# Performance work log

Hardware: AMD Instinct MI355X
Metric: run time of the kernel (lower is better)

Reference implementation:

```python
import jax, jax.numpy as jnp
import numpy as np

V, H, I, L = 32000, 1024, 2048, 4
NH, NKV, HD = 16, 8, 64
E, K = 4, 2
B, S = 2, 1024
NEG = jnp.finfo(jnp.float32).min


def setup_inputs() -> dict:
    key = jax.random.key(0)
    ks = jax.random.split(key, 11)
    w = lambda k, shape: jax.random.normal(k, shape, jnp.float32) * 0.02
    return dict(
        input_ids=jax.random.randint(ks[0], (B, S), 0, V),
        embed=w(ks[1], (V, H)),
        Wq=w(ks[2], (L, H, NH * HD)),
        Wk=w(ks[3], (L, H, NKV * HD)),
        Wv=w(ks[4], (L, H, NKV * HD)),
        Wo=w(ks[5], (L, NH * HD, H)),
        ln1=jnp.ones((L, H), jnp.float32),
        ln2=jnp.ones((L, H), jnp.float32),
        gate=w(ks[6], (L, H, E)),
        Wg=w(ks[7], (L, E, H, I)),
        Wu=w(ks[8], (L, E, H, I)),
        Wd=w(ks[9], (L, E, I, H)),
        norm_w=jnp.ones((H,), jnp.float32),
        lm_head=w(ks[10], (H, V)),
    )


def rmsnorm(x, w, eps=1e-6):
    var = jnp.mean(x * x, axis=-1, keepdims=True)
    return w * (x * jax.lax.rsqrt(var + eps))


def forward(input_ids, embed, Wq, Wk, Wv, Wo, ln1, ln2, gate, Wg, Wu, Wd, norm_w, lm_head):
    b, s = input_ids.shape
    h = embed[input_ids]  # [B,S,H]
    mask = jnp.where(jnp.triu(jnp.ones((s, s), bool), 1), NEG, 0.0)[None, None]  # causal [1,1,S,S]
    inv_sqrt_hd = 1.0 / np.sqrt(HD)
    rep = NH // NKV

    def step(h, p):
        wq, wk, wv, wo, l1, l2, gw, wg, wu, wd = p
        x = rmsnorm(h, l1)
        q = (x @ wq).reshape(b, s, NH, HD).transpose(0, 2, 1, 3)    # [B,NH,S,HD]
        k = (x @ wk).reshape(b, s, NKV, HD).transpose(0, 2, 1, 3)   # [B,NKV,S,HD]
        v = (x @ wv).reshape(b, s, NKV, HD).transpose(0, 2, 1, 3)
        k = jnp.repeat(k, rep, axis=1)  # GQA repeat_kv
        v = jnp.repeat(v, rep, axis=1)
        scores = jnp.einsum('bhqd,bhkd->bhqk', q, k) * inv_sqrt_hd + mask
        attn = jax.nn.softmax(scores, axis=-1)
        o = jnp.einsum('bhqk,bhkd->bhqd', attn, v).transpose(0, 2, 1, 3).reshape(b, s, NH * HD)
        h = h + o @ wo
        # MoE FFN (top-k routing, combine via per-expert gate weights)
        x = rmsnorm(h, l2).reshape(b * s, H)              # [T,H]
        probs = jax.nn.softmax(x @ gw, axis=-1)           # [T,E]
        topk_p, topk_i = jax.lax.top_k(probs, K)          # [T,K]
        comb = jnp.sum(topk_p[..., None] * jax.nn.one_hot(topk_i, E, dtype=x.dtype), axis=1)  # [T,E]
        g = jax.nn.silu(jnp.einsum('th,ehi->eti', x, wg))  # [E,T,I]
        u = jnp.einsum('th,ehi->eti', x, wu)
        eo = jnp.einsum('eti,eih->eth', g * u, wd)         # [E,T,H]
        moe = jnp.einsum('eth,te->th', eo, comb).reshape(b, s, H)
        return h + moe, None

    h, _ = jax.lax.scan(step, h, (Wq, Wk, Wv, Wo, ln1, ln2, gate, Wg, Wu, Wd))
    return rmsnorm(h, norm_w) @ lm_head  # [B,S,V]


def reference(input_ids, embed, Wq, Wk, Wv, Wo, ln1, ln2, gate, Wg, Wu, Wd, norm_w, lm_head):
    return forward(input_ids, embed, Wq, Wk, Wv, Wo, ln1, ln2, gate, Wg, Wu, Wd, norm_w, lm_head)
```

## Files before the change

kernel.cpp:

```cpp
#include <hip/hip_runtime.h>

#define T_ 2048
#define H_ 1024
#define S_ 1024
#define V_ 32000
#define I_ 2048
#define NHD 1024
#define KVD 512

typedef unsigned short u16;
typedef unsigned int u32;
typedef __attribute__((ext_vector_type(8))) short s16x8;
typedef __attribute__((ext_vector_type(4))) float f32x4;

__device__ __forceinline__ u16 f2b(float f){ u32 x=__builtin_bit_cast(u32,f); return (u16)((x+0x7fffu+((x>>16)&1u))>>16); }
__device__ __forceinline__ float b2f(u16 u){ return __builtin_bit_cast(float,(u32)u<<16); }
__device__ __forceinline__ float wsum(float v){ for(int o=32;o;o>>=1) v+=__shfl_xor(v,o); return v; }

__device__ __forceinline__ void gl16(const void* g, void* l){
  __builtin_amdgcn_global_load_lds(
      (const __attribute__((address_space(1))) unsigned int*)g,
      (__attribute__((address_space(3))) unsigned int*)l, 16, 0, 0);
}

__global__ void k_embed(const int* __restrict__ ids, const float* __restrict__ emb,
                        float* __restrict__ h, int* __restrict__ cnt){
  if(blockIdx.x==0 && threadIdx.x<16) cnt[threadIdx.x]=0;
  int t = blockIdx.x;
  long src = (long)ids[t]*H_;
  ((float4*)(h + (long)t*H_))[threadIdx.x] = ((const float4*)(emb+src))[threadIdx.x];
}

__global__ void k_rms_sp(const float* __restrict__ h, const float* __restrict__ w,
                         u16* __restrict__ xhi, u16* __restrict__ xlo){
  int wid = threadIdx.x>>6, lane = threadIdx.x&63;
  int t = blockIdx.x*4 + wid;
  const float* row = h + (long)t*H_;
  float v[16]; float ss=0.f;
  #pragma unroll
  for(int j=0;j<16;j++){ v[j]=row[j*64+lane]; ss += v[j]*v[j]; }
  ss = wsum(ss);
  float rstd = rsqrtf(ss/(float)H_ + 1e-6f);
  #pragma unroll
  for(int j=0;j<16;j++){
    int idx=j*64+lane;
    float y = v[j]*rstd*w[idx];
    u16 hv = f2b(y);
    xhi[(long)t*H_+idx] = hv;
    if(xlo) xlo[(long)t*H_+idx] = f2b(y - b2f(hv));
  }
}

__global__ void k_router(const float* __restrict__ h, const float* __restrict__ lw,
                         const float* __restrict__ gate, float* __restrict__ comb,
                         int* __restrict__ lists, int* __restrict__ cnt, int2* __restrict__ epos,
                         u16* __restrict__ xhi, u16* __restrict__ xlo){
  int wid = threadIdx.x>>6, lane = threadIdx.x&63;
  int t = blockIdx.x*4+wid;
  const float* row = h + (long)t*H_;
  float v[16]; float ss=0.f;
  #pragma unroll
  for(int j=0;j<16;j++){ v[j]=row[j*64+lane]; ss+=v[j]*v[j]; }
  ss = wsum(ss);
  float rstd = rsqrtf(ss/(float)H_+1e-6f);
  float a0=0,a1=0,a2=0,a3=0;
  #pragma unroll
  for(int j=0;j<16;j++){
    int idx=j*64+lane;
    float y = v[j]*rstd*lw[idx];
    u16 hv = f2b(y);
    xhi[(long)t*H_+idx] = hv;
    xlo[(long)t*H_+idx] = f2b(y - b2f(hv));
    float4 g4 = ((const float4*)gate)[idx];
    a0 += y*g4.x; a1 += y*g4.y; a2 += y*g4.z; a3 += y*g4.w;
  }
  a0=wsum(a0); a1=wsum(a1); a2=wsum(a2); a3=wsum(a3);
  if(lane==0){
    float p[4]={a0,a1,a2,a3};
    float m = fmaxf(fmaxf(p[0],p[1]),fmaxf(p[2],p[3]));
    float s=0; for(int e=0;e<4;e++){ p[e]=__expf(p[e]-m); s+=p[e]; }
    for(int e=0;e<4;e++) p[e]/=s;
    int i1=0; for(int e=1;e<4;e++) if(p[e]>p[i1]) i1=e;
    int i2=-1; for(int e=0;e<4;e++){ if(e==i1) continue; if(i2<0||p[e]>p[i2]) i2=e; }
    float* c = comb + (long)t*4;
    for(int e=0;e<4;e++) c[e] = (e==i1||e==i2)? p[e] : 0.f;
    int p1 = atomicAdd(&cnt[i1],1); lists[i1*T_+p1]=t;
    int p2 = atomicAdd(&cnt[i2],1); lists[i2*T_+p2]=t;
    epos[t] = make_int2((p1<<2)|i1, (p2<<2)|i2);
  }
}

__global__ void k_transpose(const float* __restrict__ in, u16* __restrict__ hi, u16* __restrict__ lo,
                            int R, int C, long zi, long zo){
  __shared__ float tile[32][33];
  in += (long)blockIdx.z*zi; hi += (long)blockIdx.z*zo; if(lo) lo += (long)blockIdx.z*zo;
  int c0 = blockIdx.x*32, r0 = blockIdx.y*32;
  int tx = threadIdx.x, ty = threadIdx.y;
  #pragma unroll
  for(int i=0;i<4;i++) tile[ty+8*i][tx] = in[(long)(r0+ty+8*i)*C + c0+tx];
  __syncthreads();
  #pragma unroll
  for(int i=0;i<4;i++){
    int cc=ty+8*i; float v = tile[tx][cc];
    u16 hv = f2b(v);
    long idx = (long)(c0+cc)*R + r0+tx;
    hi[idx] = hv;
    if(lo) lo[idx] = f2b(v - b2f(hv));
  }
}

__global__ void k_wtrans(const float* __restrict__ Wq, const float* __restrict__ Wk,
                         const float* __restrict__ Wv, const float* __restrict__ Wo,
                         const float* __restrict__ Wg, const float* __restrict__ Wu,
                         const float* __restrict__ Wd,
                         u16* __restrict__ qkvh, u16* __restrict__ qkvl,
                         u16* __restrict__ oh, u16* __restrict__ ol,
                         u16* __restrict__ gh, u16* __restrict__ gl_,
                         u16* __restrict__ uh, u16* __restrict__ ul,
                         u16* __restrict__ dh, u16* __restrict__ dl)
{
  __shared__ float tile[32][33];
  int id = blockIdx.x;
  const float* in; u16 *hi, *lo; int R, C, bx, by;
  if(id < 1024){ in=Wq; hi=qkvh; lo=qkvl; R=1024; C=1024; bx=id&31; by=id>>5; }
  else if(id < 1536){ id-=1024; in=Wk; hi=qkvh+1048576; lo=qkvl+1048576; R=1024; C=512; bx=id&15; by=id>>4; }
  else if(id < 2048){ id-=1536; in=Wv; hi=qkvh+1572864; lo=qkvl+1572864; R=1024; C=512; bx=id&15; by=id>>4; }
  else if(id < 3072){ id-=2048; in=Wo; hi=oh; lo=ol; R=1024; C=1024; bx=id&31; by=id>>5; }
  else if(id < 11264){ id-=3072; int z=id>>11, r2=id&2047;
    in=Wg+(size_t)z*H_*I_; hi=gh+(size_t)z*I_*H_; lo=gl_+(size_t)z*I_*H_;
    R=1024; C=2048; bx=r2&63; by=r2>>6; }
  else if(id < 19456){ id-=11264; int z=id>>11, r2=id&2047;
    in=Wu+(size_t)z*H_*I_; hi=uh+(size_t)z*I_*H_; lo=ul+(size_t)z*I_*H_;
    R=1024; C=2048; bx=r2&63; by=r2>>6; }
  else { id-=19456; int z=id>>11, r2=id&2047;
    in=Wd+(size_t)z*I_*H_; hi=dh+(size_t)z*H_*I_; lo=dl+(size_t)z*H_*I_;
    R=2048; C=1024; bx=r2&31; by=r2>>5; }
  int c0=bx*32, r0=by*32, tx=threadIdx.x, ty=threadIdx.y;
  #pragma unroll
  for(int i=0;i<4;i++) tile[ty+8*i][tx] = in[(long)(r0+ty+8*i)*C + c0+tx];
  __syncthreads();
  #pragma unroll
  for(int i=0;i<4;i++){
    int cc=ty+8*i; float v = tile[tx][cc];
    u16 hv = f2b(v);
    long idx = (long)(c0+cc)*R + r0+tx;
    hi[idx] = hv;
    lo[idx] = f2b(v - b2f(hv));
  }
}

__global__ void k_combine(float* __restrict__ h, const float* __restrict__ eo,
                          const int2* __restrict__ epos, const float* __restrict__ comb,
                          const float* __restrict__ wn, u16* __restrict__ xhi, u16* __restrict__ xlo){
  int t = blockIdx.x, c = threadIdx.x;
  int lane = c&63, wid = c>>6;
  int2 ep = epos[t];
  int e1 = ep.x&3, p1 = ep.x>>2, e2 = ep.y&3, p2 = ep.y>>2;
  float c1 = comb[t*4+e1], c2 = comb[t*4+e2];
  float4 a = ((const float4*)(eo + (long)(e1*T_+p1)*H_))[c];
  float4 b = ((const float4*)(eo + (long)(e2*T_+p2)*H_))[c];
  float4* hp = (float4*)(h + (long)t*H_) + c;
  float4 hv = *hp;
  hv.x += c1*a.x + c2*b.x; hv.y += c1*a.y + c2*b.y;
  hv.z += c1*a.z + c2*b.z; hv.w += c1*a.w + c2*b.w;
  *hp = hv;
  __shared__ float red[4];
  float ss = hv.x*hv.x + hv.y*hv.y + hv.z*hv.z + hv.w*hv.w;
  ss = wsum(ss);
  if(lane==0) red[wid]=ss;
  __syncthreads();
  float tot = red[0]+red[1]+red[2]+red[3];
  float rstd = rsqrtf(tot*(1.f/1024.f) + 1e-6f);
  float4 wv = ((const float4*)wn)[c];
  float y0=hv.x*rstd*wv.x, y1=hv.y*rstd*wv.y, y2=hv.z*rstd*wv.z, y3=hv.w*rstd*wv.w;
  ushort4 Hv; Hv.x=f2b(y0); Hv.y=f2b(y1); Hv.z=f2b(y2); Hv.w=f2b(y3);
  ((ushort4*)(xhi + (long)t*H_))[c] = Hv;
  if(xlo){
    ushort4 Lv;
    Lv.x=f2b(y0-b2f(Hv.x)); Lv.y=f2b(y1-b2f(Hv.y));
    Lv.z=f2b(y2-b2f(Hv.z)); Lv.w=f2b(y3-b2f(Hv.w));
    ((ushort4*)(xlo + (long)t*H_))[c] = Lv;
  }
}

__global__ __launch_bounds__(512) void k_flash(
  const u16* __restrict__ qh_g, const u16* __restrict__ ql_g,
  const u16* __restrict__ kh_g, const u16* __restrict__ kl_g,
  const u16* __restrict__ vth_g, const u16* __restrict__ vtl_g,
  u16* __restrict__ oh_g, u16* __restrict__ ol_g)
{
  __shared__ alignas(16) u16 Kh[8192], Kl[8192];
  __shared__ alignas(16) u16 Vh[8192], Vl[8192];
  __shared__ alignas(16) u16 Ph[16384], Pl[16384];
  const int qt = blockIdx.x, hh = blockIdx.y, b = blockIdx.z;
  const int hk = hh>>1;
  const int lane = threadIdx.x&63, w = threadIdx.x>>6;
  const int rA = lane&15, kg = (lane>>4)*8;

  s16x8 qfh[2], qfl[2];
  {
    long t = (long)(b*1024+qt*128) + w*16 + rA;
    const u16* qp = qh_g + t*NHD + hh*64;
    const u16* qp2= ql_g + t*NHD + hh*64;
    qfh[0]=*(const s16x8*)(qp + kg);      qfh[1]=*(const s16x8*)(qp + 32 + kg);
    qfl[0]=*(const s16x8*)(qp2 + kg);     qfl[1]=*(const s16x8*)(qp2 + 32 + kg);
  }

  const int ktend = qt+1;
  {
    const u16* kp = kh_g + ((long)(b*1024))*KVD + hk*64;
    const u16* kp2= kl_g + ((long)(b*1024))*KVD + hk*64;
    #pragma unroll
    for(int s=0;s<2;s++){
      int idx=s*8+w, hf=idx>>3, g=idx&7;
      int row = g*16 + (lane>>2);
      int c8  = hf*32 + (lane&3)*8;
      gl16(kp  + (long)row*KVD + c8, &Kh[hf*4096 + g*512]);
      gl16(kp2 + (long)row*KVD + c8, &Kl[hf*4096 + g*512]);
    }
  }

  f32x4 Oa[4];
  float mrun[4], lrun[4];
  #pragma unroll
  for(int jn=0;jn<4;jn++){ f32x4 zv={0.f,0.f,0.f,0.f}; Oa[jn]=zv; }
  #pragma unroll
  for(int r=0;r<4;r++){ mrun[r]=-3.0e38f; lrun[r]=0.f; }

  __syncthreads();

  for(int kt=0; kt<ktend; kt++){
    {
      const u16* vp = vth_g + (long)b*((long)KVD*S_) + (long)(hk*64)*S_ + kt*128;
      const u16* vp2= vtl_g + (long)b*((long)KVD*S_) + (long)(hk*64)*S_ + kt*128;
      #pragma unroll
      for(int s=0;s<2;s++){
        int idx=s*8+w, ks=idx>>2, g=idx&3;
        int dr = g*16 + (lane>>2);
        int k8 = (lane&3)*8;
        gl16(vp  + (long)dr*S_ + ks*32 + k8, &Vh[ks*2048 + g*512]);
        gl16(vp2 + (long)dr*S_ + ks*32 + k8, &Vl[ks*2048 + g*512]);
      }
    }

    f32x4 Sf[8];
    #pragma unroll
    for(int j=0;j<8;j++){ f32x4 zv={0.f,0.f,0.f,0.f}; Sf[j]=zv; }
    #pragma unroll
    for(int k2=0;k2<2;k2++){
      s16x8 bh[8],bl[8];
      #pragma unroll
      for(int j=0;j<8;j++){
        int ky = j*16+rA;
        bh[j]=*(const s16x8*)&Kh[k2*4096 + ky*32 + kg];
        bl[j]=*(const s16x8*)&Kl[k2*4096 + ky*32 + kg];
      }
      #pragma unroll
      for(int j=0;j<8;j++){
        Sf[j]=__builtin_amdgcn_mfma_f32_16x16x32_bf16(qfh[k2],bh[j],Sf[j],0,0,0);
        Sf[j]=__builtin_amdgcn_mfma_f32_16x16x32_bf16(qfh[k2],bl[j],Sf[j],0,0,0);
        Sf[j]=__builtin_amdgcn_mfma_f32_16x16x32_bf16(qfl[k2],bh[j],Sf[j],0,0,0);
      }
    }

    const bool last = (kt==ktend-1);
    #pragma unroll
    for(int j=0;j<8;j++)
      #pragma unroll
      for(int r=0;r<4;r++){
        float sv = Sf[j][r]*0.125f;
        if(last){
          int qr = qt*128 + w*16 + ((lane>>4)<<2) + r;
          int ky = kt*128 + j*16 + (lane&15);
          if(ky>qr) sv = -3.0e38f;
        }
        Sf[j][r]=sv;
      }

    float mt[4];
    #pragma unroll
    for(int r=0;r<4;r++){
      float v = Sf[0][r];
      #pragma unroll
      for(int j=1;j<8;j++) v = fmaxf(v, Sf[j][r]);
      v=fmaxf(v,__shfl_xor(v,1)); v=fmaxf(v,__shfl_xor(v,2));
      v=fmaxf(v,__shfl_xor(v,4)); v=fmaxf(v,__shfl_xor(v,8));
      mt[r]=v;
    }

    #pragma unroll
    for(int r=0;r<4;r++){
      float mo=mrun[r];
      float mn=fmaxf(mo,mt[r]);
      float al_=__expf(mo-mn);
      mrun[r]=mn;
      lrun[r]*=al_;
      #pragma unroll
      for(int jn=0;jn<4;jn++) Oa[jn][r]*=al_;
    }

    float ls[4];
    #pragma unroll
    for(int r=0;r<4;r++) ls[r]=0.f;
    #pragma unroll
    for(int j=0;j<8;j++)
      #pragma unroll
      for(int r=0;r<4;r++){
        int q  = w*16+((lane>>4)<<2)+r;
        int ky = j*16+(lane&15);
        float pv=__expf(Sf[j][r]-mrun[r]);
        ls[r]+=pv;
        u16 hv=f2b(pv);
        int a=(ky>>5)*4096 + q*32 + (ky&31);
        Ph[a]=hv; Pl[a]=f2b(pv-b2f(hv));
      }
    #pragma unroll
    for(int r=0;r<4;r++){
      float v=ls[r];
      v+=__shfl_xor(v,1); v+=__shfl_xor(v,2); v+=__shfl_xor(v,4); v+=__shfl_xor(v,8);
      lrun[r]+=v;
    }
    __syncthreads();

    if(kt+1<ktend){
      const u16* kp = kh_g + ((long)(b*1024+(kt+1)*128))*KVD + hk*64;
      const u16* kp2= kl_g + ((long)(b*1024+(kt+1)*128))*KVD + hk*64;
      #pragma unroll
      for(int s=0;s<2;s++){
        int idx=s*8+w, hf=idx>>3, g=idx&7;
        int row = g*16 + (lane>>2);
        int c8  = hf*32 + (lane&3)*8;
        gl16(kp  + (long)row*KVD + c8, &Kh[hf*4096 + g*512]);
        gl16(kp2 + (long)row*KVD + c8, &Kl[hf*4096 + g*512]);
      }
    }

    #pragma unroll
    for(int ks=0;ks<4;ks++){
      s16x8 pah,pal,vbh[4],vbl[4];
      int q = w*16+rA;
      pah=*(const s16x8*)&Ph[ks*4096 + q*32 + kg];
      pal=*(const s16x8*)&Pl[ks*4096 + q*32 + kg];
      #pragma unroll
      for(int jn=0;jn<4;jn++){
        int d = jn*16+rA;
        vbh[jn]=*(const s16x8*)&Vh[ks*2048 + d*32 + kg];
        vbl[jn]=*(const s16x8*)&Vl[ks*2048 + d*32 + kg];
      }
      #pragma unroll
      for(int jn=0;jn<4;jn++){
        Oa[jn]=__builtin_amdgcn_mfma_f32_16x16x32_bf16(pah,vbh[jn],Oa[jn],0,0,0);
        Oa[jn]=__builtin_amdgcn_mfma_f32_16x16x32_bf16(pah,vbl[jn],Oa[jn],0,0,0);
        Oa[jn]=__builtin_amdgcn_mfma_f32_16x16x32_bf16(pal,vbh[jn],Oa[jn],0,0,0);
      }
    }
    __syncthreads();
  }

  #pragma unroll
  for(int jn=0;jn<4;jn++)
    #pragma unroll
    for(int r=0;r<4;r++){
      long t = (long)b*1024 + qt*128 + w*16+((lane>>4)<<2)+r;
      int col = hh*64 + jn*16 + (lane&15);
      float ov = Oa[jn][r] / lrun[r];
      u16 hv=f2b(ov);
      oh_g[t*NHD+col]=hv;
      ol_g[t*NHD+col]=f2b(ov-b2f(hv));
    }
}

__global__ __launch_bounds__(256) void k_qkv(
  const u16* __restrict__ xhi, const u16* __restrict__ xlo,
  const u16* __restrict__ Bh, const u16* __restrict__ Bl,
  u16* __restrict__ qhi, u16* __restrict__ qlo,
  u16* __restrict__ khi, u16* __restrict__ klo,
  u16* __restrict__ vthi, u16* __restrict__ vtlo)
{
  __shared__ alignas(16) u16 As[2*128*64], Bs[2*128*64];
  const int m0=blockIdx.x*128, n0=blockIdx.y*128;
  const int tid=threadIdx.x, lane=tid&63, w=tid>>6, wr=w>>1, wc=w&1;
  const int rsub = lane>>3;
  const int col8 = ((lane&7) ^ (rsub&7))*8;
  const int kq = lane>>4;
  f32x4 acc[4][4];
  #pragma unroll
  for(int i=0;i<4;i++)
    #pragma unroll
    for(int j=0;j<4;j++){ f32x4 zv={0.f,0.f,0.f,0.f}; acc[i][j]=zv; }

  for(int kt=0;kt<16;kt++){
    const int k0=kt*64;
    __syncthreads();
    #pragma unroll
    for(int s=0;s<4;s++){
      int ch=s*4+w; int row=ch*8+rsub;
      gl16(xhi + (long)(m0+row)*H_ + k0+col8, &As[ch*512]);
      gl16(xlo + (long)(m0+row)*H_ + k0+col8, &As[8192+ch*512]);
      gl16(Bh  + (long)(n0+row)*H_ + k0+col8, &Bs[ch*512]);
      gl16(Bl  + (long)(n0+row)*H_ + k0+col8, &Bs[8192+ch*512]);
    }
    __syncthreads();
    #pragma unroll
    for(int ks=0;ks<2;ks++){
      s16x8 ah[4],al[4],bh[4],bl[4];
      #pragma unroll
      for(int i=0;i<4;i++){
        int row = wr*64+i*16+(lane&15);
        int sl = ((ks*4+kq) ^ (row&7))*8;
        ah[i]=*(const s16x8*)&As[row*64+sl];
        al[i]=*(const s16x8*)&As[8192+row*64+sl];
      }
      #pragma unroll
      for(int j=0;j<4;j++){
        int row = wc*64+j*16+(lane&15);
        int sl = ((ks*4+kq) ^ (row&7))*8;
        bh[j]=*(const s16x8*)&Bs[row*64+sl];
        bl[j]=*(const s16x8*)&Bs[8192+row*64+sl];
      }
      #pragma unroll
      for(int i=0;i<4;i++)
        #pragma unroll
        for(int j=0;j<4;j++){
          acc[i][j]=__builtin_amdgcn_mfma_f32_16x16x32_bf16(ah[i],bh[j],acc[i][j],0,0,0);
          acc[i][j]=__builtin_amdgcn_mfma_f32_16x16x32_bf16(ah[i],bl[j],acc[i][j],0,0,0);
          acc[i][j]=__builtin_amdgcn_mfma_f32_16x16x32_bf16(al[i],bh[j],acc[i][j],0,0,0);
        }
    }
  }

  #pragma unroll
  for(int i=0;i<4;i++){
    #pragma unroll
    for(int j=0;j<4;j++){
      const int gm0 = m0 + wr*64 + i*16 + ((lane>>4)<<2);
      const int gn  = n0 + wc*64 + j*16 + (lane&15);
      #pragma unroll
      for(int r=0;r<4;r++){
        const int gm = gm0+r;
        float v = acc[i][j][r];
        u16 hv = f2b(v);
        u16 lv = f2b(v - b2f(hv));
        if(gn < 1024){
          long idx=(long)gm*NHD+gn; qhi[idx]=hv; qlo[idx]=lv;
        } else if(gn < 1536){
          long idx=(long)gm*KVD+(gn-1024); khi[idx]=hv; klo[idx]=lv;
        } else {
          long idx=((long)(gm>>10)<<19) + (long)(gn-1536)*S_ + (gm&1023);
          vthi[idx]=hv; vtlo[idx]=lv;
        }
      }
    }
  }
}

__global__ __launch_bounds__(256) void k_moe_ug(
  const u16* __restrict__ xhi, const u16* __restrict__ xlo,
  const u16* __restrict__ Wuh, const u16* __restrict__ Wul,
  const u16* __restrict__ Wgh, const u16* __restrict__ Wgl,
  u16* __restrict__ guh, u16* __restrict__ gul,
  const int* __restrict__ lists, const int* __restrict__ cntp)
{
  const int bb = blockIdx.x;
  const int xcd = bb&7, bidx = bb>>3;
  const int grp = xcd + 8*(bidx>>4);
  const int mslot = bidx&15;
  const int e = grp>>5;
  const int n0 = (grp&31)*64;
  const int m0 = mslot*128;
  const int ce = cntp[e];
  if(m0>=ce) return;
  const int* ridx = lists + e*T_;
  const u16* Buh_g = Wuh + (size_t)e*H_*I_;
  const u16* Bul_g = Wul + (size_t)e*H_*I_;
  const u16* Bgh_g = Wgh + (size_t)e*H_*I_;
  const u16* Bgl_g = Wgl + (size_t)e*H_*I_;
  __shared__ alignas(16) u16 Ah[128*64], Al[128*64];
  __shared__ alignas(16) u16 Buh[64*64], Bul[64*64], Bgh[64*64], Bgl[64*64];
  const int tid=threadIdx.x, lane=tid&63, w=tid>>6;
  const int wr=w>>1, wc=w&1;
  const int rsub = lane>>3;
  const int col8 = ((lane&7) ^ (rsub&7))*8;
  const int kq = lane>>4;
  int arA[4];
  #pragma unroll
  for(int s=0;s<4;s++){ int idx=m0 + (s*4+w)*8 + rsub; arA[s]=ridx[idx<ce?idx:ce-1]; }
  f32x4 au[4][2], ag[4][2];
  #pragma unroll
  for(int i=0;i<4;i++)
    #pragma unroll
    for(int j=0;j<2;j++){ f32x4 zv={0.f,0.f,0.f,0.f}; au[i][j]=zv; ag[i][j]=zv; }

  for(int kt=0;kt<16;kt++){
    const int k0=kt*64;
    __syncthreads();
    #pragma unroll
    for(int s=0;s<4;s++){
      int ch=s*4+w;
      gl16(xhi + (long)arA[s]*H_ + k0+col8, &Ah[ch*512]);
      gl16(xlo + (long)arA[s]*H_ + k0+col8, &Al[ch*512]);
    }
    #pragma unroll
    for(int s=0;s<2;s++){
      int ch=s*4+w;
      int brow = n0 + ch*8 + rsub;
      gl16(Buh_g + (long)brow*H_ + k0+col8, &Buh[ch*512]);
      gl16(Bul_g + (long)brow*H_ + k0+col8, &Bul[ch*512]);
      gl16(Bgh_g + (long)brow*H_ + k0+col8, &Bgh[ch*512]);
      gl16(Bgl_g + (long)brow*H_ + k0+col8, &Bgl[ch*512]);
    }
    __syncthreads();
    #pragma unroll
    for(int ks=0;ks<2;ks++){
      s16x8 fah[4],fal[4],fbuh[2],fbul[2],fbgh[2],fbgl[2];
      #pragma unroll
      for(int i=0;i<4;i++){
        int row = wr*64+i*16+(lane&15);
        int sl = ((ks*4+kq) ^ (row&7))*8;
        fah[i]=*(const s16x8*)&Ah[row*64+sl];
        fal[i]=*(const s16x8*)&Al[row*64+sl];
      }
      #pragma unroll
      for(int j=0;j<2;j++){
        int row = wc*32+j*16+(lane&15);
        int sl = ((ks*4+kq) ^ (row&7))*8;
        fbuh[j]=*(const s16x8*)&Buh[row*64+sl];
        fbul[j]=*(const s16x8*)&Bul[row*64+sl];
        fbgh[j]=*(const s16x8*)&Bgh[row*64+sl];
        fbgl[j]=*(const s16x8*)&Bgl[row*64+sl];
      }
      #pragma unroll
      for(int i=0;i<4;i++)
        #pragma unroll
        for(int j=0;j<2;j++){
          au[i][j]=__builtin_amdgcn_mfma_f32_16x16x32_bf16(fah[i],fbuh[j],au[i][j],0,0,0);
          au[i][j]=__builtin_amdgcn_mfma_f32_16x16x32_bf16(fah[i],fbul[j],au[i][j],0,0,0);
          au[i][j]=__builtin_amdgcn_mfma_f32_16x16x32_bf16(fal[i],fbuh[j],au[i][j],0,0,0);
          ag[i][j]=__builtin_amdgcn_mfma_f32_16x16x32_bf16(fah[i],fbgh[j],ag[i][j],0,0,0);
          ag[i][j]=__builtin_amdgcn_mfma_f32_16x16x32_bf16(fah[i],fbgl[j],ag[i][j],0,0,0);
          ag[i][j]=__builtin_amdgcn_mfma_f32_16x16x32_bf16(fal[i],fbgh[j],ag[i][j],0,0,0);
        }
    }
  }

  #pragma unroll
  for(int i=0;i<4;i++){
    #pragma unroll
    for(int j=0;j<2;j++){
      const int gm0 = m0 + wr*64 + i*16 + ((lane>>4)<<2);
      const int gn  = n0 + wc*32 + j*16 + (lane&15);
      #pragma unroll
      for(int r=0;r<4;r++){
        const int gm = gm0+r;
        if(gm<ce){
          float uu=au[i][j][r], gg=ag[i][j][r];
          float val = (gg/(1.f+__expf(-gg)))*uu;
          long idx = (long)(e*T_+gm)*I_ + gn;
          u16 hv=f2b(val);
          guh[idx]=hv; gul[idx]=f2b(val-b2f(hv));
        }
      }
    }
  }
}

__global__ __launch_bounds__(512) void k_lmhead(
  const u16* __restrict__ A, const u16* __restrict__ B, float* __restrict__ C)
{
  __shared__ alignas(16) u16 smem[65536];
  const int bb = blockIdx.x;
  const int wid = (bb&7)*125 + (bb>>3);
  const int m0 = (wid&7)*256;
  const int n0 = (wid>>3)*256;
  const int tid = threadIdx.x, lane = tid&63, w = tid>>6;
  const int wr = w>>2, wc = w&3;
  const int rsub = lane>>3;
  const int col8 = ((lane&7) ^ rsub)*8;
  const int kq = lane>>4;

  f32x4 acc[8][4];
  #pragma unroll
  for(int i=0;i<8;i++)
    #pragma unroll
    for(int j=0;j<4;j++){ f32x4 zv={0.f,0.f,0.f,0.f}; acc[i][j]=zv; }

  auto stage4 = [&](int kt, int c){
    const int k0 = kt*64;
    #pragma unroll
    for(int q=0;q<4;q++){
      const u16* src = (q<2) ? A : B;
      u16* dst = &smem[(q<2 ? 0 : 32768) + c*16384 + (q&1)*8192];
      const long row0 = ((q<2) ? m0 : n0) + (q&1)*128;
      #pragma unroll
      for(int s=0;s<2;s++){
        int ch = s*8 + w;
        long row = row0 + ch*8 + rsub;
        gl16(src + row*H_ + k0 + col8, dst + ch*512);
      }
    }
  };

  stage4(0, 0);

  for(int kt=0;kt<16;kt++){
    const int c = kt&1;
    __builtin_amdgcn_s_barrier();
    __builtin_amdgcn_sched_barrier(0);
    if(kt<15) stage4(kt+1, c^1);
    __builtin_amdgcn_sched_barrier(0);
    if(kt<15) asm volatile("s_waitcnt vmcnt(8)" ::: "memory");
    else      asm volatile("s_waitcnt vmcnt(0)" ::: "memory");
    __builtin_amdgcn_sched_barrier(0);
    __builtin_amdgcn_s_barrier();
    __builtin_amdgcn_sched_barrier(0);
    #pragma unroll
    for(int ks=0;ks<2;ks++){
      s16x8 bf[4];
      #pragma unroll
      for(int j=0;j<4;j++){
        int row = wc*64 + j*16 + (lane&15);
        int sl = ((ks*4+kq) ^ (row&7))*8;
        bf[j] = *(const s16x8*)&smem[32768 + c*16384 + row*64 + sl];
      }
      #pragma unroll
      for(int ih=0;ih<2;ih++){
        s16x8 af[4];
        #pragma unroll
        for(int ii=0;ii<4;ii++){
          int row = wr*128 + (ih*4+ii)*16 + (lane&15);
          int sl = ((ks*4+kq) ^ (row&7))*8;
          af[ii] = *(const s16x8*)&smem[c*16384 + row*64 + sl];
        }
        __builtin_amdgcn_s_setprio(1);
        #pragma unroll
        for(int ii=0;ii<4;ii++)
          #pragma unroll
          for(int j=0;j<4;j++)
            acc[ih*4+ii][j] = __builtin_amdgcn_mfma_f32_16x16x32_bf16(af[ii], bf[j], acc[ih*4+ii][j], 0,0,0);
        __builtin_amdgcn_s_setprio(0);
      }
    }
  }

  float* Csf = (float*)smem;
  #pragma unroll
  for(int i=0;i<8;i++){
    __syncthreads();
    #pragma unroll
    for(int j=0;j<4;j++)
      #pragma unroll
      for(int r=0;r<4;r++)
        Csf[wr*4160 + (((lane>>4)<<2)+r)*260 + wc*64 + j*16 + (lane&15)] = acc[i][j][r];
    __syncthreads();
    const int rrow = tid>>4;
    const int wri = rrow>>4, r16 = rrow&15;
    const long gm = m0 + wri*128 + i*16 + r16;
    #pragma unroll
    for(int s=0;s<4;s++){
      int c0 = ((tid&15) + s*16)*4;
      const float* Cr = &Csf[wri*4160 + r16*260];
      float4 vv = { Cr[c0], Cr[c0+1], Cr[c0+2], Cr[c0+3] };
      *(float4*)(C + gm*(long)V_ + n0 + c0) = vv;
    }
  }
}

template<int BM,int BN,int WM,int WN,int BKT,bool SPL,int EPI,int GATH,bool SWZ,bool PIPE>
__launch_bounds__(WM*WN*64)
__global__ void k_gemm(const u16* __restrict__ Ahip, const u16* __restrict__ Alop,
                       const u16* __restrict__ Bhip, const u16* __restrict__ Blop,
                       void* __restrict__ Cp, void* __restrict__ auxp,
                       const int* __restrict__ cntp,
                       int Kdim, int lda, int ldb, int ldc,
                       long zA, long zB, int zBdiv, long zC,
                       float scale)
{
  constexpr int NT = WM*WN*64;
  constexpr int Wv = NT/64;
  constexpr int WMT = BM/WM, WNT = BN/WN;
  constexpr int MF = WMT/16, NF = WNT/16;
  constexpr int LPR = BKT/8;
  constexpr int LR  = 64/LPR;
  constexpr int ACn = (BM/LR)/Wv;
  constexpr int BCn = (BN/LR)/Wv;
  constexpr int KS  = BKT/32;
  constexpr int ABY = (SPL?2:1)*BM*BKT*2;
  constexpr int BBY = (SPL?2:1)*BN*BKT*2;
  constexpr int STEP = ABY+BBY;
  constexpr int SBY = (PIPE?2:1)*STEP;
  constexpr int CBY = (EPI==8) ? WM*16*(BN+4)*4 : 0;
  constexpr int SMB = SBY > CBY ? SBY : CBY;
  static_assert(ACn>=1 && BCn>=1, "chunks");
  __shared__ alignas(16) char smem[SMB];
  float* Csf = (float*)smem;
  constexpr int SL = T_/BM;
  int m0, n0, eid_ = 0, cnt = 0;
  if constexpr (GATH==4){
    constexpr int NTN = H_/BN;
    const int bb = blockIdx.x;
    const int xcd = bb&7, bidx = bb>>3;
    const int grp = xcd + 8*(bidx/SL);
    const int mslot = bidx%SL;
    eid_ = grp/NTN; n0 = (grp%NTN)*BN; m0 = mslot*BM;
    cnt = cntp[eid_]; if(m0>=cnt) return;
  } else if constexpr (SWZ){
    int nx = gridDim.x;
    int l = blockIdx.y*nx + blockIdx.x;
    int q = (nx*gridDim.y)>>3;
    int wid = (l&7)*q + (l>>3);
    m0 = (wid % nx)*BM; n0 = (wid / nx)*BN;
  } else {
    m0 = blockIdx.x*BM; n0 = blockIdx.y*BN;
  }
  const int z = blockIdx.z;
  const int tid = threadIdx.x, lane = tid&63, w = tid>>6;
  const int wr = w/WN, wc = w%WN;
  const int rsub = lane/LPR;
  const int col8 = (((lane%LPR) ^ (rsub&(LPR-1))))*8;
  const int kq = lane>>4;
  const u16* Ahi = Ahip + (long)z*zA + (GATH==4 ? (long)eid_*T_*lda : 0);
  const u16* Alo = SPL ? (Alop + (long)z*zA + (GATH==4 ? (long)eid_*T_*lda : 0)) : (const u16*)nullptr;
  const u16* Bh  = Bhip + (long)(z/zBdiv)*zB + (GATH==4 ? (long)eid_*zB : 0);
  const u16* Bl  = SPL ? (Blop + (long)(z/zBdiv)*zB + (GATH==4 ? (long)eid_*zB : 0)) : (const u16*)nullptr;

  f32x4 acc[MF][NF];
  #pragma unroll
  for(int i=0;i<MF;i++)
    #pragma unroll
    for(int j=0;j<NF;j++){ f32x4 zv={0.f,0.f,0.f,0.f}; acc[i][j]=zv; }

  const int ktend = Kdim/BKT;

  auto stage = [&](int kt, int bo){
    u16* As = (u16*)(smem + bo);
    u16* Bs = (u16*)(smem + bo + ABY);
    const int k0 = kt*BKT;
    #pragma unroll
    for(int s=0;s<ACn;s++){
      int ch = s*Wv + w;
      int arow = m0 + ch*LR + rsub;
      if constexpr (GATH==4){ arow = arow < cnt ? arow : cnt-1; }
      gl16(Ahi + (long)arow*lda + k0+col8, &As[ch*512]);
      if constexpr (SPL) gl16(Alo + (long)arow*lda + k0+col8, &As[BM*BKT + ch*512]);
    }
    #pragma unroll
    for(int s=0;s<BCn;s++){
      int ch = s*Wv + w;
      int brow = n0 + ch*LR + rsub;
      gl16(Bh + (long)brow*ldb + k0+col8, &Bs[ch*512]);
      if constexpr (SPL) gl16(Bl + (long)brow*ldb + k0+col8, &Bs[BN*BKT + ch*512]);
    }
  };

  auto compute = [&](int bo){
    u16* As = (u16*)(smem + bo);
    u16* Bs = (u16*)(smem + bo + ABY);
    #pragma unroll
    for(int ks=0;ks<KS;ks++){
      s16x8 ah[MF], al[MF], bh[NF], bl[NF];
      #pragma unroll
      for(int i=0;i<MF;i++){
        int row = wr*WMT+i*16+(lane&15);
        int sl = ((ks*4+kq) ^ (row&(LPR-1)))*8;
        ah[i]=*(const s16x8*)&As[row*BKT+sl];
        if constexpr (SPL) al[i]=*(const s16x8*)&As[BM*BKT+row*BKT+sl];
      }
      #pragma unroll
      for(int j=0;j<NF;j++){
        int row = wc*WNT+j*16+(lane&15);
        int sl = ((ks*4+kq) ^ (row&(LPR-1)))*8;
        bh[j]=*(const s16x8*)&Bs[row*BKT+sl];
        if constexpr (SPL) bl[j]=*(const s16x8*)&Bs[BN*BKT+row*BKT+sl];
      }
      #pragma unroll
      for(int i=0;i<MF;i++)
        #pragma unroll
        for(int j=0;j<NF;j++){
          acc[i][j]=__builtin_amdgcn_mfma_f32_16x16x32_bf16(ah[i],bh[j],acc[i][j],0,0,0);
          if constexpr (SPL){
            acc[i][j]=__builtin_amdgcn_mfma_f32_16x16x32_bf16(ah[i],bl[j],acc[i][j],0,0,0);
            acc[i][j]=__builtin_amdgcn_mfma_f32_16x16x32_bf16(al[i],bh[j],acc[i][j],0,0,0);
          }
        }
    }
  };

  if constexpr (PIPE){
    stage(0, 0);
    __syncthreads();
    for(int kt=0;kt<ktend;kt++){
      int cur = kt&1;
      if(kt+1<ktend) stage(kt+1, (cur^1)*STEP);
      compute(cur*STEP);
      __syncthreads();
    }
  } else {
    for(int kt=0;kt<ktend;kt++){
      __syncthreads();
      stage(kt, 0);
      __syncthreads();
      compute(0);
    }
  }

  if constexpr (EPI==8){
    float* C = (float*)Cp + (long)z*zC;
    #pragma unroll
    for(int i=0;i<MF;i++){
      __syncthreads();
      #pragma unroll
      for(int j=0;j<NF;j++)
        #pragma unroll
        for(int r=0;r<4;r++)
          Csf[wr*16*(BN+4) + (((lane>>4)<<2)+r)*(BN+4) + wc*WNT + j*16 + (lane&15)] = acc[i][j][r]*scale;
      __syncthreads();
      const int rrow = tid>>3;
      const int wri = rrow>>4, r16 = rrow&15;
      const long gm = m0 + wri*WMT + i*16 + r16;
      #pragma unroll
      for(int s=0;s<BN/32;s++){
        int c0 = ((tid&7) + s*8)*4;
        const float* Cr = &Csf[wri*16*(BN+4) + r16*(BN+4)];
        float4 vv = { Cr[c0], Cr[c0+1], Cr[c0+2], Cr[c0+3] };
        *(float4*)(C + gm*ldc + n0 + c0) = vv;
      }
    }
    return;
  }

  #pragma unroll
  for(int i=0;i<MF;i++){
    #pragma unroll
    for(int j=0;j<NF;j++){
      const int gm0 = m0 + wr*WMT + i*16 + ((lane>>4)<<2);
      const int gn  = n0 + wc*WNT + j*16 + (lane&15);
      #pragma unroll
      for(int r=0;r<4;r++){
        const int gm = gm0+r;
        const float v = acc[i][j][r];
        const bool live = (GATH==0) || (gm < cnt);
        if constexpr (EPI==1){
          if(live) ((float*)Cp + (long)z*zC)[(long)gm*ldc+gn] = v*scale;
        } else if constexpr (EPI==2){
          float* C = (float*)Cp; C[(long)gm*ldc+gn] += v;
        } else if constexpr (EPI==7){
          if(live) ((float*)Cp)[(long)(eid_*T_+gm)*ldc+gn] = v*scale;
        } else if constexpr (EPI==9){
          u16* Ch = (u16*)Cp + (long)z*zC;
          u16* Cl = (u16*)auxp + (long)z*zC;
          long idx = (long)gm*ldc+gn;
          u16 hv = f2b(v);
          Ch[idx]=hv; Cl[idx]=f2b(v-b2f(hv));
        }
      }
    }
  }
}

extern "C" void kernel_launch(void* const* d_in, const int* in_sizes, int n_in,
                              void* d_out, int out_size, void* d_ws, size_t ws_size,
                              hipStream_t stream)
{
  (void)in_sizes; (void)n_in; (void)out_size;
  const int*   ids   = (const int*)d_in[0];
  const float* emb   = (const float*)d_in[1];
  const float* Wq    = (const float*)d_in[2];
  const float* Wk    = (const float*)d_in[3];
  const float* Wv    = (const float*)d_in[4];
  const float* Wo    = (const float*)d_in[5];
  const float* ln1   = (const float*)d_in[6];
  const float* ln2   = (const float*)d_in[7];
  const float* gate  = (const float*)d_in[8];
  const float* Wg    = (const float*)d_in[9];
  const float* Wu    = (const float*)d_in[10];
  const float* Wd    = (const float*)d_in[11];
  const float* normw = (const float*)d_in[12];
  const float* lmh   = (const float*)d_in[13];

  char* p = (char*)d_ws;
  auto carve = [&](size_t bytes)->void*{ void* r=p; p += (bytes+255)&~(size_t)255; return r; };
  float* h    = (float*)carve((size_t)T_*H_*4);
  u16*   xhi  = (u16*)  carve((size_t)T_*H_*2);
  u16*   xlo  = (u16*)  carve((size_t)T_*H_*2);
  u16*   qhi  = (u16*)  carve((size_t)T_*NHD*2);
  u16*   qlo  = (u16*)  carve((size_t)T_*NHD*2);
  u16*   khi  = (u16*)  carve((size_t)T_*KVD*2);
  u16*   klo  = (u16*)  carve((size_t)T_*KVD*2);
  u16*   vthi = (u16*)  carve((size_t)T_*KVD*2);
  u16*   vtlo = (u16*)  carve((size_t)T_*KVD*2);
  u16*   ohi  = (u16*)  carve((size_t)T_*NHD*2);
  u16*   olo  = (u16*)  carve((size_t)T_*NHD*2);
  float* comb = (float*)carve((size_t)T_*4*4);
  int*   cnt  = (int*)  carve((size_t)16*4);
  int*   lists= (int*)  carve((size_t)4*T_*4);
  int2*  epos = (int2*) carve((size_t)T_*8);
  char*  U    = (char*) carve((size_t)112*1024*1024);
  u16*   wp   = (u16*)  carve((size_t)56623104*2);
  if ((size_t)(p - (char*)d_ws) > ws_size) return;

  u16*   guh  = (u16*)U;
  u16*   gul  = (u16*)(U + 33554432);
  float* eo   = (float*)(U + 67108864);

  u16 *WqkvTh = wp,          *WqkvTl = wp+2097152;
  u16 *WoTh = wp+4194304,    *WoTl = wp+5242880;
  u16 *WgTh = wp+6291456,    *WgTl = wp+14680064;
  u16 *WuTh = wp+23068672,   *WuTl = wp+31457280;
  u16 *WdTh = wp+39845888,   *WdTl = wp+48234496;

  dim3 tb(32,8);

  k_embed<<<T_,256,0,stream>>>(ids, emb, h, cnt);

  for(int l=0;l<4;l++){
    k_wtrans<<<27648,tb,0,stream>>>(
      Wq+(size_t)l*H_*NHD, Wk+(size_t)l*H_*KVD, Wv+(size_t)l*H_*KVD, Wo+(size_t)l*NHD*H_,
      Wg+(size_t)l*4*H_*I_, Wu+(size_t)l*4*H_*I_, Wd+(size_t)l*4*I_*H_,
      WqkvTh, WqkvTl, WoTh, WoTl, WgTh, WgTl, WuTh, WuTl, WdTh, WdTl);

    if(l==0) k_rms_sp<<<T_/4,256,0,stream>>>(h, ln1, xhi, xlo);

    k_qkv<<<dim3(16,16),256,0,stream>>>(xhi, xlo, WqkvTh, WqkvTl, qhi, qlo, khi, klo, vthi, vtlo);

    k_flash<<<dim3(8,16,2),512,0,stream>>>(qhi, qlo, khi, klo, vthi, vtlo, ohi, olo);

    k_gemm<64,128,2,2,64,true,2,0,false,false><<<dim3(32,8,1),256,0,stream>>>(
      ohi, olo, WoTh, WoTl, h, nullptr, nullptr, NHD, NHD, NHD, H_, 0,0,1,0, 0.f);

    k_router<<<T_/4,256,0,stream>>>(h, ln2+(size_t)l*H_, gate+(size_t)l*H_*4, comb, lists, cnt+l*4, epos, xhi, xlo);

    k_moe_ug<<<2048,256,0,stream>>>(xhi, xlo, WuTh, WuTl, WgTh, WgTl, guh, gul, lists, cnt+l*4);
    k_gemm<128,128,2,2,64,true,7,4,false,false><<<512,256,0,stream>>>(
      guh, gul, WdTh, WdTl, eo, nullptr, cnt+l*4, I_, I_, I_, H_, 0, (long)I_*H_, 1, 0, 1.f);
    if(l<3)
      k_combine<<<T_,256,0,stream>>>(h, eo, epos, comb, ln1+(size_t)(l+1)*H_, xhi, xlo);
    else
      k_combine<<<T_,256,0,stream>>>(h, eo, epos, comb, normw, xhi, nullptr);
  }

  k_transpose<<<dim3(1000,32),tb,0,stream>>>(lmh, wp, nullptr, H_, V_, 0,0);
  k_lmhead<<<1000,512,0,stream>>>(xhi, wp, (float*)d_out);
}
```

Before: 1.843 ms.

## Double-buffer LDS in MoE up/gate and down GEMMs with vmcnt-based prefetch

```diff
diff --git a/kernel.cpp b/kernel.cpp
--- a/kernel.cpp
+++ b/kernel.cpp
@@ -475,8 +475,7 @@
   const u16* Bul_g = Wul + (size_t)e*H_*I_;
   const u16* Bgh_g = Wgh + (size_t)e*H_*I_;
   const u16* Bgl_g = Wgl + (size_t)e*H_*I_;
-  __shared__ alignas(16) u16 Ah[128*64], Al[128*64];
-  __shared__ alignas(16) u16 Buh[64*64], Bul[64*64], Bgh[64*64], Bgl[64*64];
+  __shared__ alignas(16) u16 smem[65536];
   const int tid=threadIdx.x, lane=tid&63, w=tid>>6;
   const int wr=w>>1, wc=w&1;
   const int rsub = lane>>3;
@@ -491,25 +490,40 @@
     #pragma unroll
     for(int j=0;j<2;j++){ f32x4 zv={0.f,0.f,0.f,0.f}; au[i][j]=zv; ag[i][j]=zv; }
 
-  for(int kt=0;kt<16;kt++){
-    const int k0=kt*64;
-    __syncthreads();
+  auto stage = [&](int kt, int c){
+    const int k0 = kt*64;
+    u16* base = &smem[c*32768];
     #pragma unroll
     for(int s=0;s<4;s++){
       int ch=s*4+w;
-      gl16(xhi + (long)arA[s]*H_ + k0+col8, &Ah[ch*512]);
-      gl16(xlo + (long)arA[s]*H_ + k0+col8, &Al[ch*512]);
+      gl16(xhi + (long)arA[s]*H_ + k0+col8, base + ch*512);
+      gl16(xlo + (long)arA[s]*H_ + k0+col8, base + 8192 + ch*512);
     }
     #pragma unroll
     for(int s=0;s<2;s++){
       int ch=s*4+w;
       int brow = n0 + ch*8 + rsub;
-      gl16(Buh_g + (long)brow*H_ + k0+col8, &Buh[ch*512]);
-      gl16(Bul_g + (long)brow*H_ + k0+col8, &Bul[ch*512]);
-      gl16(Bgh_g + (long)brow*H_ + k0+col8, &Bgh[ch*512]);
-      gl16(Bgl_g + (long)brow*H_ + k0+col8, &Bgl[ch*512]);
-    }
-    __syncthreads();
+      gl16(Buh_g + (long)brow*H_ + k0+col8, base + 16384 + ch*512);
+      gl16(Bul_g + (long)brow*H_ + k0+col8, base + 20480 + ch*512);
+      gl16(Bgh_g + (long)brow*H_ + k0+col8, base + 24576 + ch*512);
+      gl16(Bgl_g + (long)brow*H_ + k0+col8, base + 28672 + ch*512);
+    }
+  };
+
+  stage(0, 0);
+
+  for(int kt=0;kt<16;kt++){
+    const int c = kt&1;
+    __builtin_amdgcn_s_barrier();
+    __builtin_amdgcn_sched_barrier(0);
+    if(kt<15) stage(kt+1, c^1);
+    __builtin_amdgcn_sched_barrier(0);
+    if(kt<15) asm volatile("s_waitcnt vmcnt(16)" ::: "memory");
+    else      asm volatile("s_waitcnt vmcnt(0)" ::: "memory");
+    __builtin_amdgcn_sched_barrier(0);
+    __builtin_amdgcn_s_barrier();
+    __builtin_amdgcn_sched_barrier(0);
+    const u16* base = &smem[c*32768];
     #pragma unroll
     for(int ks=0;ks<2;ks++){
       s16x8 fah[4],fal[4],fbuh[2],fbul[2],fbgh[2],fbgl[2];
@@ -517,18 +531,19 @@
       for(int i=0;i<4;i++){
         int row = wr*64+i*16+(lane&15);
         int sl = ((ks*4+kq) ^ (row&7))*8;
-        fah[i]=*(const s16x8*)&Ah[row*64+sl];
-        fal[i]=*(const s16x8*)&Al[row*64+sl];
+        fah[i]=*(const s16x8*)&base[row*64+sl];
+        fal[i]=*(const s16x8*)&base[8192+row*64+sl];
       }
       #pragma unroll
       for(int j=0;j<2;j++){
         int row = wc*32+j*16+(lane&15);
         int sl = ((ks*4+kq) ^ (row&7))*8;
-        fbuh[j]=*(const s16x8*)&Buh[row*64+sl];
-        fbul[j]=*(const s16x8*)&Bul[row*64+sl];
-        fbgh[j]=*(const s16x8*)&Bgh[row*64+sl];
-        fbgl[j]=*(const s16x8*)&Bgl[row*64+sl];
-      }
+        fbuh[j]=*(const s16x8*)&base[16384+row*64+sl];
+        fbul[j]=*(const s16x8*)&base[20480+row*64+sl];
+        fbgh[j]=*(const s16x8*)&base[24576+row*64+sl];
+        fbgl[j]=*(const s16x8*)&base[28672+row*64+sl];
+      }
+      __builtin_amdgcn_s_setprio(1);
       #pragma unroll
       for(int i=0;i<4;i++)
         #pragma unroll
@@ -540,6 +555,7 @@
           ag[i][j]=__builtin_amdgcn_mfma_f32_16x16x32_bf16(fah[i],fbgl[j],ag[i][j],0,0,0);
           ag[i][j]=__builtin_amdgcn_mfma_f32_16x16x32_bf16(fal[i],fbgh[j],ag[i][j],0,0,0);
         }
+      __builtin_amdgcn_s_setprio(0);
     }
   }
 
@@ -665,7 +681,7 @@
   }
 }
 
-template<int BM,int BN,int WM,int WN,int BKT,bool SPL,int EPI,int GATH,bool SWZ,bool PIPE>
+template<int BM,int BN,int WM,int WN,int BKT,bool SPL,int EPI,int GATH,bool SWZ,bool CNT>
 __launch_bounds__(WM*WN*64)
 __global__ void k_gemm(const u16* __restrict__ Ahip, const u16* __restrict__ Alop,
                        const u16* __restrict__ Bhip, const u16* __restrict__ Blop,
@@ -687,7 +703,9 @@
   constexpr int ABY = (SPL?2:1)*BM*BKT*2;
   constexpr int BBY = (SPL?2:1)*BN*BKT*2;
   constexpr int STEP = ABY+BBY;
-  constexpr int SBY = (PIPE?2:1)*STEP;
+  constexpr int NLD = (ACn+BCn)*(SPL?2:1);
+  static_assert(!CNT || NLD==16, "CNT schedule hardcodes vmcnt(16)");
+  constexpr int SBY = (CNT?2:1)*STEP;
   constexpr int CBY = (EPI==8) ? WM*16*(BN+4)*4 : 0;
   constexpr int SMB = SBY > CBY ? SBY : CBY;
   static_assert(ACn>=1 && BCn>=1, "chunks");
@@ -785,14 +803,20 @@
     }
   };
 
-  if constexpr (PIPE){
+  if constexpr (CNT){
     stage(0, 0);
-    __syncthreads();
     for(int kt=0;kt<ktend;kt++){
-      int cur = kt&1;
+      const int cur = kt&1;
+      __builtin_amdgcn_s_barrier();
+      __builtin_amdgcn_sched_barrier(0);
       if(kt+1<ktend) stage(kt+1, (cur^1)*STEP);
+      __builtin_amdgcn_sched_barrier(0);
+      if(kt+1<ktend) asm volatile("s_waitcnt vmcnt(16)" ::: "memory");
+      else           asm volatile("s_waitcnt vmcnt(0)" ::: "memory");
+      __builtin_amdgcn_sched_barrier(0);
+      __builtin_amdgcn_s_barrier();
+      __builtin_amdgcn_sched_barrier(0);
       compute(cur*STEP);
-      __syncthreads();
     }
   } else {
     for(int kt=0;kt<ktend;kt++){
@@ -930,7 +954,7 @@
     k_router<<<T_/4,256,0,stream>>>(h, ln2+(size_t)l*H_, gate+(size_t)l*H_*4, comb, lists, cnt+l*4, epos, xhi, xlo);
 
     k_moe_ug<<<2048,256,0,stream>>>(xhi, xlo, WuTh, WuTl, WgTh, WgTl, guh, gul, lists, cnt+l*4);
-    k_gemm<128,128,2,2,64,true,7,4,false,false><<<512,256,0,stream>>>(
+    k_gemm<128,128,2,2,64,true,7,4,false,true><<<512,256,0,stream>>>(
       guh, gul, WdTh, WdTl, eo, nullptr, cnt+l*4, I_, I_, I_, H_, 0, (long)I_*H_, 1, 0, 1.f);
     if(l<3)
       k_combine<<<T_,256,0,stream>>>(h, eo, epos, comb, ln1+(size_t)(l+1)*H_, xhi, xlo);
```

Measured after the change: 2.076 ms. +12.7%, slower.
